# Performance work log

Hardware: AMD Instinct MI355X
Metric: run time of the kernel (lower is better)

Reference implementation:

```python
import jax, jax.numpy as jnp
import numpy as np

BS, NA, NT, ED, AD, NC = 64, 900, 600, 256, 11, 10
CONF_DECAY = 0.6


def _topk_gather(conf, k, *xs):
    # conf: [bs, N] -> top-k values + gather rows of each x: [bs, N, d] -> [bs, k, d]
    vals, idx = jax.lax.top_k(conf, k)
    outs = [jnp.take_along_axis(x, idx[:, :, None], axis=1) for x in xs]
    return vals, outs


def setup_inputs() -> dict:
    key = jax.random.key(0)
    ks = jax.random.split(key, 7)
    return {
        "instance_feature": jax.random.normal(ks[0], (BS, NA, ED), jnp.float32),
        "anchor": jax.random.normal(ks[1], (BS, NA, AD), jnp.float32),
        "confidence": jax.random.normal(ks[2], (BS, NA, NC), jnp.float32),
        "cached_feature": jax.random.normal(ks[3], (BS, NT, ED), jnp.float32),
        "cached_anchor": jax.random.normal(ks[4], (BS, NT, AD), jnp.float32),
        "prev_confidence": jax.random.uniform(ks[5], (BS, NT), jnp.float32),
        "mask": jax.random.bernoulli(ks[6], 0.8, (BS,)),
    }


def reference(instance_feature, anchor, confidence, cached_feature, cached_anchor, prev_confidence, mask):
    # ---- InstanceBank.update ----
    N = NA - NT  # number of fresh instances kept alongside the temporal cache
    conf_max = confidence.max(axis=-1)  # [bs, NA]
    _, (sel_f, sel_a) = _topk_gather(conf_max, N, instance_feature, anchor)
    sel_f = jnp.concatenate([cached_feature, sel_f], axis=1)  # [bs, NA, ED]
    sel_a = jnp.concatenate([cached_anchor, sel_a], axis=1)   # [bs, NA, AD]
    m = mask[:, None, None]
    feat = jnp.where(m, sel_f, instance_feature)
    anc = jnp.where(m, sel_a, anchor)

    # ---- InstanceBank.cache (detached path) ----
    conf_c = jax.nn.sigmoid(jax.lax.stop_gradient(conf_max))
    conf_c = conf_c.at[:, :NT].set(jnp.maximum(prev_confidence * CONF_DECAY, conf_c[:, :NT]))
    new_conf, (cf, ca) = _topk_gather(
        conf_c, NT, jax.lax.stop_gradient(feat), jax.lax.stop_gradient(anc)
    )

    merged = jnp.concatenate([feat, anc], axis=-1)  # [bs, NA, ED+AD]
    return merged, new_conf, cf, ca
```

## Files before the change

### kernel.cpp

```cpp
#include <hip/hip_runtime.h>

#define BS   64
#define NA   900
#define NT   600
#define NSEL 300
#define ED   256
#define AD   11
#define NC   10
#define SORTN 1024
#define CACHED_FLAG 0x40000000

#define OFF_MERGED  0
#define OFF_NEWCONF (BS * NA * (ED + AD))
#define OFF_CF      (OFF_NEWCONF + BS * NT)
#define OFF_CA      (OFF_CF + BS * NT * ED)

typedef float f32x4 __attribute__((ext_vector_type(4)));

__device__ __forceinline__ unsigned int fkey(float x) {
    unsigned int u = __float_as_uint(x);
    return (u & 0x80000000u) ? ~u : (u | 0x80000000u);
}

__device__ __forceinline__ unsigned long long shfl_xor64(unsigned long long v, int m) {
    return (unsigned long long)__shfl_xor((long long)v, m, 64);
}

__device__ __forceinline__ void sort1024(unsigned long long& key, int i,
                                         unsigned long long* lds) {
    for (int k = 2; k <= SORTN; k <<= 1) {
        for (int j = k >> 1; j > 0; j >>= 1) {
            unsigned long long partner;
            if (j >= 64) {
                __syncthreads();
                lds[i] = key;
                __syncthreads();
                partner = lds[i ^ j];
            } else {
                partner = shfl_xor64(key, j);
            }
            const bool up      = ((i & k) == 0);
            const bool lower   = ((i & j) == 0);
            const bool keepmin = (lower == up);
            const bool pgt     = (key > partner);
            key = (keepmin == pgt) ? partner : key;
        }
    }
}

__device__ __forceinline__ float conf_max_row(const float* __restrict__ confidence,
                                              int b, int i) {
    const float* cp = confidence + ((size_t)b * NA + i) * NC;
    float m = cp[0];
    #pragma unroll
    for (int k = 1; k < NC; k++) m = fmaxf(m, cp[k]);
    return m;
}

__global__ __launch_bounds__(1024) void topk_kernel(
    const float* __restrict__ confidence,
    const float* __restrict__ prev_conf,
    const int*   __restrict__ mask,
    float*       __restrict__ new_conf_out,
    int*         __restrict__ src_map,
    int*         __restrict__ pos2)
{
    __shared__ unsigned long long keys[SORTN];
    __shared__ float cc_s[NA];

    const int b = blockIdx.x >> 1;
    const int i = threadIdx.x;

    if ((blockIdx.x & 1) == 0) {
        const int mk = mask[b];
        if (!mk) {
            if (i < NA) src_map[(size_t)b * NA + i] = i;
            return;
        }
        if (i < NT) src_map[(size_t)b * NA + i] = i | CACHED_FLAG;

        float cmax = (i < NA) ? conf_max_row(confidence, b, i) : 0.0f;
        unsigned long long key = (i < NA)
            ? ((((unsigned long long)(~fkey(cmax))) << 32) | (unsigned int)i)
            : 0xFFFFFFFFFFFFFFFFull;
        sort1024(key, i, keys);
        if (i < NSEL)
            src_map[(size_t)b * NA + NT + i] = (int)(key & 0xFFFFFFFFull);
    } else {
        float c = 0.0f;
        if (i < NA) {
            float cmax = conf_max_row(confidence, b, i);
            double d = 1.0 / (1.0 + exp(-(double)cmax));
            c = (float)d;
            if (i < NT) c = fmaxf(prev_conf[(size_t)b * NT + i] * 0.6f, c);
            cc_s[i] = c;
        }
        unsigned long long key = (i < NA)
            ? ((((unsigned long long)(~fkey(c))) << 32) | (unsigned int)i)
            : 0xFFFFFFFFFFFFFFFFull;
        sort1024(key, i, keys);
        if (i < NT) {
            int r = (int)(key & 0xFFFFFFFFull);
            new_conf_out[(size_t)b * NT + i] = cc_s[r];
            pos2[(size_t)b * NA + r] = i;
        } else if (i < NA) {
            int r = (int)(key & 0xFFFFFFFFull);
            pos2[(size_t)b * NA + r] = -1;
        }
    }
}

__global__ __launch_bounds__(256) void gather_kernel(
    const float* __restrict__ inst_f,
    const float* __restrict__ anchor,
    const float* __restrict__ cached_f,
    const float* __restrict__ cached_a,
    const int*   __restrict__ src_map,
    const int*   __restrict__ pos2,
    float*       __restrict__ out)
{
    const int wave = threadIdx.x >> 6;
    const int lane = threadIdx.x & 63;
    const int gr   = blockIdx.x * 4 + wave;
    if (gr >= BS * NA) return;

    const int b = gr / NA;
    const int t = gr - b * NA;

    const int s = src_map[(size_t)b * NA + t];
    const int p = pos2[(size_t)b * NA + t];

    const float* fsrc;
    const float* asrc;
    if (s & CACHED_FLAG) {
        const int r = s & 0xFFFF;
        fsrc = cached_f + ((size_t)b * NT + r) * ED;
        asrc = cached_a + ((size_t)b * NT + r) * AD;
    } else {
        fsrc = inst_f + ((size_t)b * NA + s) * ED;
        asrc = anchor + ((size_t)b * NA + s) * AD;
    }

    const f32x4 v = __builtin_nontemporal_load((const f32x4*)fsrc + lane);
    float av = 0.0f;
    if (lane < AD) av = asrc[lane];

    float* orow = out + OFF_MERGED + ((size_t)b * NA + t) * (ED + AD);
    __builtin_nontemporal_store(v.x, orow + 4 * lane + 0);
    __builtin_nontemporal_store(v.y, orow + 4 * lane + 1);
    __builtin_nontemporal_store(v.z, orow + 4 * lane + 2);
    __builtin_nontemporal_store(v.w, orow + 4 * lane + 3);
    if (lane < AD) __builtin_nontemporal_store(av, orow + ED + lane);

    if (p >= 0) {
        f32x4* crow = (f32x4*)(out + OFF_CF + ((size_t)b * NT + p) * ED);
        __builtin_nontemporal_store(v, crow + lane);
        if (lane < AD)
            __builtin_nontemporal_store(av, out + OFF_CA + ((size_t)b * NT + p) * AD + lane);
    }
}

extern "C" void kernel_launch(void* const* d_in, const int* in_sizes, int n_in,
                              void* d_out, int out_size, void* d_ws, size_t ws_size,
                              hipStream_t stream) {
    const float* inst_f = (const float*)d_in[0];
    const float* anchor = (const float*)d_in[1];
    const float* conf   = (const float*)d_in[2];
    const float* cach_f = (const float*)d_in[3];
    const float* cach_a = (const float*)d_in[4];
    const float* prevc  = (const float*)d_in[5];
    const int*   mask   = (const int*)d_in[6];
    float* out = (float*)d_out;

    int* src_map = (int*)d_ws;
    int* pos2    = src_map + BS * NA;

    topk_kernel<<<2 * BS, 1024, 0, stream>>>(conf, prevc, mask,
                                             out + OFF_NEWCONF, src_map, pos2);

    const int nrows = BS * NA;
    gather_kernel<<<(nrows + 3) / 4, 256, 0, stream>>>(
        inst_f, anchor, cach_f, cach_a, src_map, pos2, out);
}
```

Baseline: 190.3 us.

## Replace bitonic sort top-k with rank-by-counting split across blocks

Replaces the 1024-element bitonic sort in the top-k kernel with a rank computation. Each element's rank is the count of larger keys, scanned from shared memory, and is used directly as the output position. The work per batch is split across 4 blocks of 256 threads per mode, so 512 smaller blocks replace 128 large ones. Each block recomputes the full confidence max and keys for all 900 rows, and the O(N^2) comparison scan trades sort barriers for redundant compute.

```diff
diff --git a/kernel.cpp b/kernel.cpp
--- a/kernel.cpp
+++ b/kernel.cpp
@@ -7,7 +7,8 @@
 #define ED   256
 #define AD   11
 #define NC   10
-#define SORTN 1024
+#define SPLIT 4
+#define RPB  (NA / SPLIT)
 #define CACHED_FLAG 0x40000000
 
 #define OFF_MERGED  0
@@ -16,36 +17,12 @@
 #define OFF_CA      (OFF_CF + BS * NT * ED)
 
 typedef float f32x4 __attribute__((ext_vector_type(4)));
+typedef unsigned long long u64;
+typedef u64 u64x2 __attribute__((ext_vector_type(2)));
 
 __device__ __forceinline__ unsigned int fkey(float x) {
     unsigned int u = __float_as_uint(x);
     return (u & 0x80000000u) ? ~u : (u | 0x80000000u);
-}
-
-__device__ __forceinline__ unsigned long long shfl_xor64(unsigned long long v, int m) {
-    return (unsigned long long)__shfl_xor((long long)v, m, 64);
-}
-
-__device__ __forceinline__ void sort1024(unsigned long long& key, int i,
-                                         unsigned long long* lds) {
-    for (int k = 2; k <= SORTN; k <<= 1) {
-        for (int j = k >> 1; j > 0; j >>= 1) {
-            unsigned long long partner;
-            if (j >= 64) {
-                __syncthreads();
-                lds[i] = key;
-                __syncthreads();
-                partner = lds[i ^ j];
-            } else {
-                partner = shfl_xor64(key, j);
-            }
-            const bool up      = ((i & k) == 0);
-            const bool lower   = ((i & j) == 0);
-            const bool keepmin = (lower == up);
-            const bool pgt     = (key > partner);
-            key = (keepmin == pgt) ? partner : key;
-        }
-    }
 }
 
 __device__ __forceinline__ float conf_max_row(const float* __restrict__ confidence,
@@ -57,7 +34,7 @@
     return m;
 }
 
-__global__ __launch_bounds__(1024) void topk_kernel(
+__global__ __launch_bounds__(256) void topk_kernel(
     const float* __restrict__ confidence,
     const float* __restrict__ prev_conf,
     const int*   __restrict__ mask,
@@ -65,47 +42,72 @@
     int*         __restrict__ src_map,
     int*         __restrict__ pos2)
 {
-    __shared__ unsigned long long keys[SORTN];
+    __shared__ __align__(16) u64 w_s[NA];
     __shared__ float cc_s[NA];
 
-    const int b = blockIdx.x >> 1;
-    const int i = threadIdx.x;
+    const int bid  = blockIdx.x;
+    const int b    = bid & (BS - 1);
+    const int p    = bid >> 6;
+    const int mode = p >> 2;
+    const int part = p & (SPLIT - 1);
+    const int t    = threadIdx.x;
 
-    if ((blockIdx.x & 1) == 0) {
+    if (mode == 0) {
         const int mk = mask[b];
         if (!mk) {
-            if (i < NA) src_map[(size_t)b * NA + i] = i;
+            const int base = part * RPB;
+            if (t < RPB) src_map[(size_t)b * NA + base + t] = base + t;
             return;
         }
-        if (i < NT) src_map[(size_t)b * NA + i] = i | CACHED_FLAG;
-
-        float cmax = (i < NA) ? conf_max_row(confidence, b, i) : 0.0f;
-        unsigned long long key = (i < NA)
-            ? ((((unsigned long long)(~fkey(cmax))) << 32) | (unsigned int)i)
-            : 0xFFFFFFFFFFFFFFFFull;
-        sort1024(key, i, keys);
-        if (i < NSEL)
-            src_map[(size_t)b * NA + NT + i] = (int)(key & 0xFFFFFFFFull);
+        {
+            const int base = part * (NT / SPLIT);
+            if (t < NT / SPLIT)
+                src_map[(size_t)b * NA + base + t] = (base + t) | CACHED_FLAG;
+        }
+        for (int i = t; i < NA; i += 256) {
+            float m = conf_max_row(confidence, b, i);
+            w_s[i] = ((u64)fkey(m) << 32) | (unsigned int)(NA - 1 - i);
+        }
+        __syncthreads();
+        if (t < RPB) {
+            const int i = part * RPB + t;
+            const u64 wi = w_s[i];
+            const u64x2* w2 = (const u64x2*)w_s;
+            unsigned int cnt = 0;
+            #pragma unroll 10
+            for (int j = 0; j < NA / 2; ++j) {
+                const u64x2 q = w2[j];
+                cnt += (unsigned int)(q.x > wi) + (unsigned int)(q.y > wi);
+            }
+            if (cnt < NSEL)
+                src_map[(size_t)b * NA + NT + cnt] = i;
+        }
     } else {
-        float c = 0.0f;
-        if (i < NA) {
-            float cmax = conf_max_row(confidence, b, i);
-            double d = 1.0 / (1.0 + exp(-(double)cmax));
-            c = (float)d;
+        for (int i = t; i < NA; i += 256) {
+            float m = conf_max_row(confidence, b, i);
+            double d = 1.0 / (1.0 + exp(-(double)m));
+            float c = (float)d;
             if (i < NT) c = fmaxf(prev_conf[(size_t)b * NT + i] * 0.6f, c);
             cc_s[i] = c;
+            w_s[i] = ((u64)fkey(c) << 32) | (unsigned int)(NA - 1 - i);
         }
-        unsigned long long key = (i < NA)
-            ? ((((unsigned long long)(~fkey(c))) << 32) | (unsigned int)i)
-            : 0xFFFFFFFFFFFFFFFFull;
-        sort1024(key, i, keys);
-        if (i < NT) {
-            int r = (int)(key & 0xFFFFFFFFull);
-            new_conf_out[(size_t)b * NT + i] = cc_s[r];
-            pos2[(size_t)b * NA + r] = i;
-        } else if (i < NA) {
-            int r = (int)(key & 0xFFFFFFFFull);
-            pos2[(size_t)b * NA + r] = -1;
+        __syncthreads();
+        if (t < RPB) {
+            const int i = part * RPB + t;
+            const u64 wi = w_s[i];
+            const u64x2* w2 = (const u64x2*)w_s;
+            unsigned int cnt = 0;
+            #pragma unroll 10
+            for (int j = 0; j < NA / 2; ++j) {
+                const u64x2 q = w2[j];
+                cnt += (unsigned int)(q.x > wi) + (unsigned int)(q.y > wi);
+            }
+            if (cnt < NT) {
+                new_conf_out[(size_t)b * NT + cnt] = cc_s[i];
+                pos2[(size_t)b * NA + i] = (int)cnt;
+            } else {
+                pos2[(size_t)b * NA + i] = -1;
+            }
         }
     }
 }
@@ -175,8 +177,8 @@
     int* src_map = (int*)d_ws;
     int* pos2    = src_map + BS * NA;
 
-    topk_kernel<<<2 * BS, 1024, 0, stream>>>(conf, prevc, mask,
-                                             out + OFF_NEWCONF, src_map, pos2);
+    topk_kernel<<<8 * BS, 256, 0, stream>>>(conf, prevc, mask,
+                                            out + OFF_NEWCONF, src_map, pos2);
 
     const int nrows = BS * NA;
     gather_kernel<<<(nrows + 3) / 4, 256, 0, stream>>>(
```

After: 195.6 us. 1.03x slower.
